# Optimization experiments

Hardware: AMD Instinct MI355X
Metric: run time of the kernel (lower is better)

The kernel has to match this reference:

```python
import jax, jax.numpy as jnp
import numpy as np

B, L, S, D, H, NS, NSLOT = 2, 2048, 2048, 1024, 16, 8, 512
HD = D // H


def _silu(x):
    return x * jax.nn.sigmoid(x)


def _layernorm(x, g, b, eps=1e-5):
    mu = jnp.mean(x, axis=-1, keepdims=True)
    var = jnp.var(x, axis=-1, keepdims=True)
    return (x - mu) * jax.lax.rsqrt(var + eps) * g + b


def setup_inputs() -> dict:
    key = jax.random.key(0)
    ks = jax.random.split(key, 12)
    x_q = jax.random.normal(ks[0], (B, L, D), dtype=jnp.float32)
    x_idx = jax.random.randint(ks[1], (B, S), 0, NSLOT)
    E_slots = jax.random.normal(ks[2], (NSLOT, D), dtype=jnp.float32)
    # EMA decay rates close to 1 so multi-scale gates stay non-degenerate over S steps
    rhos = 1.0 - 0.005 * jax.random.uniform(ks[3], (NS,), dtype=jnp.float32)
    C_seq = jax.random.uniform(ks[4], (B, L, NS), dtype=jnp.float32)
    s = 1.0 / np.sqrt(D)
    Wq = jax.random.normal(ks[5], (D, D), dtype=jnp.float32) * s
    Wk = jax.random.normal(ks[6], (D, D), dtype=jnp.float32) * s
    Wv = jax.random.normal(ks[7], (D, D), dtype=jnp.float32) * s
    Wo = jax.random.normal(ks[8], (D, D), dtype=jnp.float32) * s
    Wpe = jax.random.normal(ks[9], (D, NS), dtype=jnp.float32) * (1.0 / np.sqrt(NS))
    ln_kv_g = jnp.ones((D,), jnp.float32); ln_kv_b = jnp.zeros((D,), jnp.float32)
    ln_q_g = jnp.ones((D,), jnp.float32); ln_q_b = jnp.zeros((D,), jnp.float32)
    return dict(x_q=x_q, x_idx=x_idx, E_slots=E_slots, rhos=rhos, C_seq=C_seq,
                Wq=Wq, Wk=Wk, Wv=Wv, Wo=Wo, Wpe=Wpe,
                ln_kv_g=ln_kv_g, ln_kv_b=ln_kv_b, ln_q_g=ln_q_g, ln_q_b=ln_q_b)


def reference(x_q, x_idx, E_slots, rhos, C_seq, Wq, Wk, Wv, Wo, Wpe,
              ln_kv_g, ln_kv_b, ln_q_g, ln_q_b):
    # --- KV side: memory = ln_kv(E_slots); K/V = proj(memory); gather by slot id ---
    mem = _layernorm(E_slots, ln_kv_g, ln_kv_b)          # [NSLOT, D]
    Ek = mem @ Wk.T                                       # [NSLOT, D]
    Ev = mem @ Wv.T
    K = Ek[x_idx]                                         # [B, S, D] embedding lookup
    V = Ev[x_idx]
    # --- multiplicative EMA gate per kv position: c[s,m] = rho_m^(age) ---
    ages = (S - 1 - jnp.arange(S)).astype(x_q.dtype)      # [S]
    c_kv = jnp.power(rhos[None, :], ages[:, None])        # [S, NS]
    gate_kv = _silu(c_kv @ Wpe.T)                         # [S, D] = SiLU(pe_proj(C))
    K = K * gate_kv[None]
    V = V * gate_kv[None]
    # --- symmetric query gating: Q = q_proj(ln_q(x_q * SiLU(pe_proj(C_seq)))) ---
    gate_q = _silu(C_seq @ Wpe.T)                         # [B, L, D]
    Q = _layernorm(x_q * gate_q, ln_q_g, ln_q_b) @ Wq.T   # [B, L, D]
    # --- multi-head softmax attention ---
    q = Q.reshape(B, L, H, HD)
    k = K.reshape(B, S, H, HD)
    v = V.reshape(B, S, H, HD)
    scores = jnp.einsum('blhd,bshd->bhls', q, k) / np.sqrt(HD).astype(np.float32)
    attn = jax.nn.softmax(scores, axis=-1)                # [B, H, L, S]
    out = jnp.einsum('bhls,bshd->blhd', attn, v).reshape(B, L, D)
    return out @ Wo.T                                     # o_proj (dropout = identity, eval)
```

## Files before the change

kernel.cpp:

```cpp
#include <hip/hip_runtime.h>
#include <cmath>
#include <cstddef>

namespace {

constexpr int cB = 2, cL = 2048, cS = 2048, cD = 1024, cH = 16, cNS = 8, cNSLOT = 512, cHD = 64;

typedef __attribute__((ext_vector_type(8))) short short8;
typedef __attribute__((ext_vector_type(4))) float f32x4;

#define MFMA16(a, b, c) __builtin_amdgcn_mfma_f32_16x16x32_bf16((a), (b), (c), 0, 0, 0)

__device__ __forceinline__ float sigmoidf_(float x) { return 1.f / (1.f + __expf(-x)); }

__device__ __forceinline__ unsigned short f2bf(float x) {
  union { float f; unsigned u; } c; c.f = x;
  unsigned r = c.u + 0x7FFFu + ((c.u >> 16) & 1u);
  return (unsigned short)(r >> 16);
}
__device__ __forceinline__ float bf2f(unsigned short h) {
  union { unsigned u; float f; } c; c.u = ((unsigned)h) << 16;
  return c.f;
}

__device__ __forceinline__ void async16(const void* g, void* l) {
  __builtin_amdgcn_global_load_lds((const __attribute__((address_space(1))) void*)g,
                                   (__attribute__((address_space(3))) void*)l, 16, 0, 0);
}

__global__ __launch_bounds__(256) void prep_all_kernel(
    const float* __restrict__ Wq, const float* __restrict__ Wk,
    const float* __restrict__ Wv, const float* __restrict__ Wo,
    unsigned short* __restrict__ Wqh, unsigned short* __restrict__ Wql,
    unsigned short* __restrict__ Wkh, unsigned short* __restrict__ Wkl,
    unsigned short* __restrict__ Wvh, unsigned short* __restrict__ Wvl,
    unsigned short* __restrict__ Woh, unsigned short* __restrict__ Wol,
    const float* __restrict__ E, const float* __restrict__ lnkv_g,
    const float* __restrict__ lnkv_b, unsigned short* __restrict__ mh,
    unsigned short* __restrict__ ml, const float* __restrict__ rhos,
    const float* __restrict__ Wpe, float* __restrict__ gkv,
    const float* __restrict__ xq, const float* __restrict__ Cseq,
    const float* __restrict__ lnq_g, const float* __restrict__ lnq_b,
    unsigned short* __restrict__ Yh, unsigned short* __restrict__ Yl) {
  __shared__ float sC[cNS];
  __shared__ float rbuf[8];
  const int bid = blockIdx.x;
  const int tid = threadIdx.x;

  if (bid < 2048) {
    const int wid = bid >> 9;
    const size_t off = ((size_t)(bid & 511) * 256 + tid) * 8;
    const float* src = wid == 0 ? Wq : wid == 1 ? Wk : wid == 2 ? Wv : Wo;
    unsigned short* dh = wid == 0 ? Wqh : wid == 1 ? Wkh : wid == 2 ? Wvh : Woh;
    unsigned short* dl = wid == 0 ? Wql : wid == 1 ? Wkl : wid == 2 ? Wvl : Wol;
    const float4 a = *(const float4*)(src + off);
    const float4 b = *(const float4*)(src + off + 4);
    float v[8] = {a.x, a.y, a.z, a.w, b.x, b.y, b.z, b.w};
    unsigned short h8[8], l8[8];
#pragma unroll
    for (int j = 0; j < 8; j++) {
      h8[j] = f2bf(v[j]);
      l8[j] = f2bf(v[j] - bf2f(h8[j]));
    }
    *(uint4*)(dh + off) = *(uint4*)h8;
    *(uint4*)(dl + off) = *(uint4*)l8;
  } else if (bid < 2560) {
    const int row = bid - 2048;
    const int d0 = tid * 4;
    const float4 x = *(const float4*)(E + (size_t)row * cD + d0);
    float s1 = x.x + x.y + x.z + x.w;
    float s2 = x.x * x.x + x.y * x.y + x.z * x.z + x.w * x.w;
#pragma unroll
    for (int o = 32; o > 0; o >>= 1) { s1 += __shfl_xor(s1, o, 64); s2 += __shfl_xor(s2, o, 64); }
    if ((tid & 63) == 0) { rbuf[tid >> 6] = s1; rbuf[4 + (tid >> 6)] = s2; }
    __syncthreads();
    s1 = rbuf[0] + rbuf[1] + rbuf[2] + rbuf[3];
    s2 = rbuf[4] + rbuf[5] + rbuf[6] + rbuf[7];
    const float mean = s1 * (1.f / cD);
    const float var = s2 * (1.f / cD) - mean * mean;
    const float inv = rsqrtf(var + 1e-5f);
    const float4 g = *(const float4*)(lnkv_g + d0);
    const float4 b = *(const float4*)(lnkv_b + d0);
    float y[4];
    y[0] = (x.x - mean) * inv * g.x + b.x;
    y[1] = (x.y - mean) * inv * g.y + b.y;
    y[2] = (x.z - mean) * inv * g.z + b.z;
    y[3] = (x.w - mean) * inv * g.w + b.w;
    unsigned short h4[4], l4[4];
#pragma unroll
    for (int j = 0; j < 4; j++) {
      h4[j] = f2bf(y[j]);
      l4[j] = f2bf(y[j] - bf2f(h4[j]));
    }
    *(uint2*)(mh + (size_t)row * cD + d0) = *(uint2*)h4;
    *(uint2*)(ml + (size_t)row * cD + d0) = *(uint2*)l4;
  } else if (bid < 4608) {
    const int s = bid - 2560;
    if (tid < cNS) {
      const float age = (float)(cS - 1 - s);
      sC[tid] = __expf(age * __logf(rhos[tid]));
    }
    __syncthreads();
    const int d0 = tid * 4;
    float4 o4;
#pragma unroll
    for (int j = 0; j < 4; j++) {
      const float* wr = Wpe + (size_t)(d0 + j) * cNS;
      float gs = 0.f;
#pragma unroll
      for (int m = 0; m < cNS; m++) gs += sC[m] * wr[m];
      ((float*)&o4)[j] = gs * sigmoidf_(gs);
    }
    *(float4*)(gkv + (size_t)s * cD + d0) = o4;
  } else {
    const int row = bid - 4608;
    if (tid < cNS) sC[tid] = Cseq[(size_t)row * cNS + tid];
    __syncthreads();
    const int d0 = tid * 4;
    const float4 x = *(const float4*)(xq + (size_t)row * cD + d0);
    float y[4];
    float s1 = 0.f, s2 = 0.f;
#pragma unroll
    for (int j = 0; j < 4; j++) {
      const float* wr = Wpe + (size_t)(d0 + j) * cNS;
      float gs = 0.f;
#pragma unroll
      for (int m = 0; m < cNS; m++) gs += sC[m] * wr[m];
      const float val = ((const float*)&x)[j] * gs * sigmoidf_(gs);
      y[j] = val;
      s1 += val;
      s2 += val * val;
    }
#pragma unroll
    for (int o = 32; o > 0; o >>= 1) { s1 += __shfl_xor(s1, o, 64); s2 += __shfl_xor(s2, o, 64); }
    if ((tid & 63) == 0) { rbuf[tid >> 6] = s1; rbuf[4 + (tid >> 6)] = s2; }
    __syncthreads();
    s1 = rbuf[0] + rbuf[1] + rbuf[2] + rbuf[3];
    s2 = rbuf[4] + rbuf[5] + rbuf[6] + rbuf[7];
    const float mean = s1 * (1.f / cD);
    const float var = s2 * (1.f / cD) - mean * mean;
    const float inv = rsqrtf(var + 1e-5f);
    const float4 g = *(const float4*)(lnq_g + d0);
    const float4 b = *(const float4*)(lnq_b + d0);
    float z[4];
    z[0] = (y[0] - mean) * inv * g.x + b.x;
    z[1] = (y[1] - mean) * inv * g.y + b.y;
    z[2] = (y[2] - mean) * inv * g.z + b.z;
    z[3] = (y[3] - mean) * inv * g.w + b.w;
    unsigned short h4[4], l4[4];
#pragma unroll
    for (int j = 0; j < 4; j++) {
      h4[j] = f2bf(z[j]);
      l4[j] = f2bf(z[j] - bf2f(h4[j]));
    }
    *(uint2*)(Yh + (size_t)row * cD + d0) = *(uint2*)h4;
    *(uint2*)(Yl + (size_t)row * cD + d0) = *(uint2*)l4;
  }
}

template <int MODE>
__global__ __launch_bounds__(256, 2) void gemm_sp_kernel(
    const unsigned short* __restrict__ Ahi, const unsigned short* __restrict__ Alo,
    const unsigned short* __restrict__ Whi0, const unsigned short* __restrict__ Wlo0,
    const unsigned short* __restrict__ Whi1, const unsigned short* __restrict__ Wlo1,
    float* __restrict__ Cf0, float* __restrict__ Cf1,
    unsigned short* __restrict__ Chi,
    int M, int N, int K, float scale) {
  __shared__ __align__(16) unsigned short sAh[2][128 * 32];
  __shared__ __align__(16) unsigned short sAl[2][128 * 32];
  __shared__ __align__(16) unsigned short sBh[2][64 * 32];
  __shared__ __align__(16) unsigned short sBl[2][64 * 32];
  const unsigned short* Whi = blockIdx.z ? Whi1 : Whi0;
  const unsigned short* Wlo = blockIdx.z ? Wlo1 : Wlo0;
  float* Cf = blockIdx.z ? Cf1 : Cf0;
  const int tid = threadIdx.x;
  const int wave = tid >> 6, lane = tid & 63;
  const int quad = lane >> 4, l16 = lane & 15;
  const int m0 = blockIdx.y * 128, n0 = blockIdx.x * 64;
  const int wy = wave >> 1, wx = wave & 1;
  const int sg = (lane & 3) ^ ((lane >> 3) & 3);
  const int srow = lane >> 2;

  f32x4 acc[4][2];
#pragma unroll
  for (int i = 0; i < 4; i++)
#pragma unroll
    for (int j = 0; j < 2; j++) acc[i][j] = (f32x4){0.f, 0.f, 0.f, 0.f};

  auto stage = [&](int buf, int k0) {
#pragma unroll
    for (int c = 0; c < 2; c++) {
      const int row = c * 64 + wave * 16 + srow;
      const size_t ga = (size_t)(m0 + row) * K + k0 + sg * 8;
      async16(Ahi + ga, &sAh[buf][(c * 64 + wave * 16) * 32]);
      async16(Alo + ga, &sAl[buf][(c * 64 + wave * 16) * 32]);
    }
    const int rowb = wave * 16 + srow;
    const size_t gb = (size_t)(n0 + rowb) * K + k0 + sg * 8;
    async16(Whi + gb, &sBh[buf][wave * 16 * 32]);
    async16(Wlo + gb, &sBl[buf][wave * 16 * 32]);
  };

  stage(0, 0);
  __syncthreads();
  const int aswz = (l16 >> 1) & 3;
  int buf = 0;
  for (int k0 = 0; k0 < K; k0 += 32, buf ^= 1) {
    if (k0 + 32 < K) stage(buf ^ 1, k0 + 32);
    short8 bh[2], bl2[2];
#pragma unroll
    for (int tj = 0; tj < 2; tj++) {
      const int br = (wx * 32 + tj * 16 + l16) * 32 + ((quad ^ aswz) * 8);
      bh[tj] = *(const short8*)&sBh[buf][br];
      bl2[tj] = *(const short8*)&sBl[buf][br];
    }
#pragma unroll
    for (int ti = 0; ti < 4; ti++) {
      const int ar = (wy * 64 + ti * 16 + l16) * 32 + ((quad ^ aswz) * 8);
      const short8 ah = *(const short8*)&sAh[buf][ar];
      const short8 al2 = *(const short8*)&sAl[buf][ar];
#pragma unroll
      for (int tj = 0; tj < 2; tj++) {
        acc[ti][tj] = MFMA16(ah, bh[tj], acc[ti][tj]);
        acc[ti][tj] = MFMA16(al2, bh[tj], acc[ti][tj]);
        acc[ti][tj] = MFMA16(ah, bl2[tj], acc[ti][tj]);
      }
    }
    __syncthreads();
  }

#pragma unroll
  for (int ti = 0; ti < 4; ti++)
#pragma unroll
    for (int tj = 0; tj < 2; tj++) {
      const int row = m0 + wy * 64 + ti * 16 + quad * 4;
      const int col = n0 + wx * 32 + tj * 16 + l16;
#pragma unroll
      for (int r = 0; r < 4; r++) {
        const size_t idx = (size_t)(row + r) * N + col;
        if constexpr (MODE == 0) {
          Cf[idx] = acc[ti][tj][r];
        } else {
          Chi[idx] = f2bf(acc[ti][tj][r] * scale);
        }
      }
    }
}

__global__ __launch_bounds__(256) void prep_kv_kernel(
    const float* __restrict__ Ek, const float* __restrict__ Ev,
    const float* __restrict__ gkv, const int* __restrict__ xidx,
    unsigned short* __restrict__ Khi, unsigned short* __restrict__ Vthi) {
  __shared__ float tile[64][65];
  const int bid = blockIdx.x;
  const int tid = threadIdx.x;
  if (bid < 2048) {
    const int t = bid * 256 + tid;
    const int d0 = (t & 127) * 8;
    const int s = (t >> 7) & (cS - 1);
    const int b = t >> 18;
    const int slot = xidx[b * cS + s];
    const float4 e0 = *(const float4*)(Ek + (size_t)slot * cD + d0);
    const float4 e1 = *(const float4*)(Ek + (size_t)slot * cD + d0 + 4);
    const float4 g0 = *(const float4*)(gkv + (size_t)s * cD + d0);
    const float4 g1 = *(const float4*)(gkv + (size_t)s * cD + d0 + 4);
    float v[8] = {e0.x * g0.x, e0.y * g0.y, e0.z * g0.z, e0.w * g0.w,
                  e1.x * g1.x, e1.y * g1.y, e1.z * g1.z, e1.w * g1.w};
    unsigned short h8[8];
#pragma unroll
    for (int j = 0; j < 8; j++) h8[j] = f2bf(v[j]);
    *(uint4*)(Khi + (size_t)(b * cS + s) * cD + d0) = *(uint4*)h8;
  } else {
    const int local = bid - 2048;
    const int s0 = (local & 31) * 64;
    const int d0 = ((local >> 5) & 15) * 64;
    const int b = local >> 9;
    const int sl = tid >> 4;
    const int dl = (tid & 15) * 4;
#pragma unroll
    for (int it = 0; it < 4; it++) {
      const int s = s0 + sl + it * 16;
      const int slot = xidx[b * cS + s];
      const float4 e = *(const float4*)(Ev + (size_t)slot * cD + d0 + dl);
      const float4 g = *(const float4*)(gkv + (size_t)s * cD + d0 + dl);
      tile[sl + it * 16][dl + 0] = e.x * g.x;
      tile[sl + it * 16][dl + 1] = e.y * g.y;
      tile[sl + it * 16][dl + 2] = e.z * g.z;
      tile[sl + it * 16][dl + 3] = e.w * g.w;
    }
    __syncthreads();
    const int dr = tid >> 3;
    const int sc = (tid & 7) * 8;
#pragma unroll
    for (int it = 0; it < 2; it++) {
      const int d = d0 + dr + it * 32;
      unsigned short h8[8];
#pragma unroll
      for (int j = 0; j < 8; j++) h8[j] = f2bf(tile[sc + j][dr + it * 32]);
      *(uint4*)(Vthi + (size_t)(b * cD + d) * cS + s0 + sc) = *(uint4*)h8;
    }
  }
}

__global__ __launch_bounds__(256, 4) void attn_mfma_kernel(
    const unsigned short* __restrict__ qhi,
    const unsigned short* __restrict__ Khi,
    const unsigned short* __restrict__ Vthi,
    unsigned short* __restrict__ AOhi, unsigned short* __restrict__ AOlo) {
  __shared__ __align__(16) unsigned short sKh[64 * 64];
  __shared__ __align__(16) unsigned short sVh[64 * 64];
  __shared__ __align__(16) unsigned short sP[4][16][72];

  const int tid = threadIdx.x;
  const int wave = tid >> 6, lane = tid & 63;
  const int quad = lane >> 4, l16 = lane & 15;
  const int lB = blockIdx.x * 64;
  const int h = blockIdx.y, b = blockIdx.z;

  short8 qh[2];
  {
    const size_t base = (size_t)(b * cL + lB + wave * 16 + l16) * cD + h * cHD + quad * 8;
    qh[0] = *(const short8*)(qhi + base);
    qh[1] = *(const short8*)(qhi + base + 32);
  }

  short8 ones;
#pragma unroll
  for (int i = 0; i < 8; i++) ones[i] = (short)0x3F80;

  f32x4 O[4], dacc;
#pragma unroll
  for (int i = 0; i < 4; i++) O[i] = (f32x4){0.f, 0.f, 0.f, 0.f};
  dacc = (f32x4){0.f, 0.f, 0.f, 0.f};

  const int srow8 = lane >> 3;
  const int sg = (lane & 7) ^ srow8;

  const int r0 = (wave * 2 + 0) * 8 + srow8;
  const int r1 = (wave * 2 + 1) * 8 + srow8;
  const size_t kb0 = (size_t)(b * cS + r0) * cD + h * cHD + sg * 8;
  const size_t kb1 = (size_t)(b * cS + r1) * cD + h * cHD + sg * 8;
  const size_t vb0 = (size_t)(b * cD + h * cHD + r0) * cS + sg * 8;
  const size_t vb1 = (size_t)(b * cD + h * cHD + r1) * cS + sg * 8;

  uint4 k0h, v0h, k1h, v1h;
  k0h = *(const uint4*)(Khi + kb0);
  v0h = *(const uint4*)(Vthi + vb0);
  k1h = *(const uint4*)(Khi + kb1);
  v1h = *(const uint4*)(Vthi + vb1);

  const int j0 = wave * 2, j1 = wave * 2 + 1;

  for (int s0 = 0; s0 < cS; s0 += 64) {
    __syncthreads();
    *(uint4*)&sKh[j0 * 512 + lane * 8] = k0h;
    *(uint4*)&sVh[j0 * 512 + lane * 8] = v0h;
    *(uint4*)&sKh[j1 * 512 + lane * 8] = k1h;
    *(uint4*)&sVh[j1 * 512 + lane * 8] = v1h;
    __syncthreads();

    {
      const int sn = (s0 + 64) & (cS - 1);
      const size_t kc = (size_t)sn * cD;
      k0h = *(const uint4*)(Khi + kb0 + kc);
      v0h = *(const uint4*)(Vthi + vb0 + sn);
      k1h = *(const uint4*)(Khi + kb1 + kc);
      v1h = *(const uint4*)(Vthi + vb1 + sn);
    }

    f32x4 sc[4];
#pragma unroll
    for (int st = 0; st < 4; st++) sc[st] = (f32x4){0.f, 0.f, 0.f, 0.f};
#pragma unroll
    for (int st = 0; st < 4; st++) {
      const int srw = st * 16 + l16;
#pragma unroll
      for (int ks = 0; ks < 2; ks++) {
        const int slot = (ks * 4 + quad) ^ (srw & 7);
        const short8 kfh = *(const short8*)&sKh[srw * 64 + slot * 8];
        sc[st] = MFMA16(qh[ks], kfh, sc[st]);
      }
    }

#pragma unroll
    for (int st = 0; st < 4; st++)
#pragma unroll
      for (int r = 0; r < 4; r++)
        sP[wave][quad * 4 + r][st * 16 + l16] = f2bf(__builtin_amdgcn_exp2f(sc[st][r]));

    short8 pfh[2];
    pfh[0] = *(const short8*)&sP[wave][l16][quad * 8];
    pfh[1] = *(const short8*)&sP[wave][l16][32 + quad * 8];

#pragma unroll
    for (int dt = 0; dt < 4; dt++) {
      const int drw = dt * 16 + l16;
#pragma unroll
      for (int ss = 0; ss < 2; ss++) {
        const int slot = (ss * 4 + quad) ^ (drw & 7);
        const short8 vfh = *(const short8*)&sVh[drw * 64 + slot * 8];
        O[dt] = MFMA16(pfh[ss], vfh, O[dt]);
      }
    }
    dacc = MFMA16(pfh[0], ones, dacc);
    dacc = MFMA16(pfh[1], ones, dacc);
  }

  float inv[4];
#pragma unroll
  for (int r = 0; r < 4; r++) inv[r] = 1.f / dacc[r];
#pragma unroll
  for (int dt = 0; dt < 4; dt++)
#pragma unroll
    for (int r = 0; r < 4; r++) {
      const float v = O[dt][r] * inv[r];
      const unsigned short hi = f2bf(v);
      const size_t l = (size_t)(b * cL + lB + wave * 16 + quad * 4 + r);
      const size_t idx = l * cD + h * cHD + dt * 16 + l16;
      AOhi[idx] = hi;
      AOlo[idx] = f2bf(v - bf2f(hi));
    }
}

}

extern "C" void kernel_launch(void* const* d_in, const int* in_sizes, int n_in,
                              void* d_out, int out_size, void* d_ws, size_t ws_size,
                              hipStream_t stream) {
  (void)in_sizes; (void)n_in; (void)out_size; (void)ws_size;
  const float* x_q = (const float*)d_in[0];
  const int* x_idx = (const int*)d_in[1];
  const float* E_slots = (const float*)d_in[2];
  const float* rhos = (const float*)d_in[3];
  const float* C_seq = (const float*)d_in[4];
  const float* Wq = (const float*)d_in[5];
  const float* Wk = (const float*)d_in[6];
  const float* Wv = (const float*)d_in[7];
  const float* Wo = (const float*)d_in[8];
  const float* Wpe = (const float*)d_in[9];
  const float* ln_kv_g = (const float*)d_in[10];
  const float* ln_kv_b = (const float*)d_in[11];
  const float* ln_q_g = (const float*)d_in[12];
  const float* ln_q_b = (const float*)d_in[13];
  float* out = (float*)d_out;

  float* ws = (float*)d_ws;
  unsigned short* memhi = (unsigned short*)(ws + 0);
  unsigned short* memlo = (unsigned short*)(ws + 262144);
  unsigned short* Wkhi = (unsigned short*)(ws + 524288);
  unsigned short* Wklo = (unsigned short*)(ws + 1048576);
  unsigned short* Wvhi = (unsigned short*)(ws + 1572864);
  unsigned short* Wvlo = (unsigned short*)(ws + 2097152);
  float* gkv = ws + 2621440;
  unsigned short* qhi = (unsigned short*)(ws + 0);
  unsigned short* Wqhi = (unsigned short*)(ws + 4718592);
  unsigned short* Wqlo = (unsigned short*)(ws + 5242880);
  unsigned short* Wohi = (unsigned short*)(ws + 5767168);
  unsigned short* Wolo = (unsigned short*)(ws + 6291456);
  float* Ek = ws + 6815744;
  float* Ev = ws + 7340032;
  unsigned short* Yhi = (unsigned short*)(ws + 7864320);
  unsigned short* Ylo = (unsigned short*)(ws + 9961472);
  unsigned short* AOhi = (unsigned short*)(ws + 7864320);
  unsigned short* AOlo = (unsigned short*)(ws + 9961472);
  unsigned short* Khi = (unsigned short*)(ws + 12058624);
  unsigned short* Vthi = (unsigned short*)(ws + 16252928);

  constexpr float kQScale = 0.125f * 1.44269504088896340736f;

  prep_all_kernel<<<8704, 256, 0, stream>>>(
      Wq, Wk, Wv, Wo, Wqhi, Wqlo, Wkhi, Wklo, Wvhi, Wvlo, Wohi, Wolo,
      E_slots, ln_kv_g, ln_kv_b, memhi, memlo, rhos, Wpe, gkv,
      x_q, C_seq, ln_q_g, ln_q_b, Yhi, Ylo);
  gemm_sp_kernel<0><<<dim3(16, 4, 2), 256, 0, stream>>>(
      memhi, memlo, Wkhi, Wklo, Wvhi, Wvlo, Ek, Ev, nullptr, cNSLOT, cD, cD, 1.f);
  prep_kv_kernel<<<3072, 256, 0, stream>>>(Ek, Ev, gkv, x_idx, Khi, Vthi);
  gemm_sp_kernel<1><<<dim3(16, 32, 1), 256, 0, stream>>>(
      Yhi, Ylo, Wqhi, Wqlo, Wqhi, Wqlo, nullptr, nullptr, qhi, cB * cL, cD, cD, kQScale);
  attn_mfma_kernel<<<dim3(cL / 64, cH, cB), 256, 0, stream>>>(qhi, Khi, Vthi, AOhi, AOlo);
  gemm_sp_kernel<0><<<dim3(16, 32, 1), 256, 0, stream>>>(
      AOhi, AOlo, Wohi, Wolo, Wohi, Wolo, out, out, nullptr, cB * cL, cD, cD, 1.f);
}
```

Measured before the change: 296.1 us.

## Drop activation low-part split in GEMMs and double query rows per attention wave

Activations (layernormed memory, Q input, attention output) are now stored only as a bf16 high part. The GEMMs drop the A-low operand: one fewer MFMA per tile, half the A staging traffic and less LDS. The attention kernel now processes 32 query rows per wave (128 per block), reusing each K/V LDS fragment for two query tiles, with occupancy lowered to 2. Accuracy falls because activations lose the error-compensation term.

```diff
diff --git a/kernel.cpp b/kernel.cpp
--- a/kernel.cpp
+++ b/kernel.cpp
@@ -37,11 +37,11 @@
     unsigned short* __restrict__ Woh, unsigned short* __restrict__ Wol,
     const float* __restrict__ E, const float* __restrict__ lnkv_g,
     const float* __restrict__ lnkv_b, unsigned short* __restrict__ mh,
-    unsigned short* __restrict__ ml, const float* __restrict__ rhos,
+    const float* __restrict__ rhos,
     const float* __restrict__ Wpe, float* __restrict__ gkv,
     const float* __restrict__ xq, const float* __restrict__ Cseq,
     const float* __restrict__ lnq_g, const float* __restrict__ lnq_b,
-    unsigned short* __restrict__ Yh, unsigned short* __restrict__ Yl) {
+    unsigned short* __restrict__ Yh) {
   __shared__ float sC[cNS];
   __shared__ float rbuf[8];
   const int bid = blockIdx.x;
@@ -81,19 +81,12 @@
     const float inv = rsqrtf(var + 1e-5f);
     const float4 g = *(const float4*)(lnkv_g + d0);
     const float4 b = *(const float4*)(lnkv_b + d0);
-    float y[4];
-    y[0] = (x.x - mean) * inv * g.x + b.x;
-    y[1] = (x.y - mean) * inv * g.y + b.y;
-    y[2] = (x.z - mean) * inv * g.z + b.z;
-    y[3] = (x.w - mean) * inv * g.w + b.w;
-    unsigned short h4[4], l4[4];
-#pragma unroll
-    for (int j = 0; j < 4; j++) {
-      h4[j] = f2bf(y[j]);
-      l4[j] = f2bf(y[j] - bf2f(h4[j]));
-    }
+    unsigned short h4[4];
+    h4[0] = f2bf((x.x - mean) * inv * g.x + b.x);
+    h4[1] = f2bf((x.y - mean) * inv * g.y + b.y);
+    h4[2] = f2bf((x.z - mean) * inv * g.z + b.z);
+    h4[3] = f2bf((x.w - mean) * inv * g.w + b.w);
     *(uint2*)(mh + (size_t)row * cD + d0) = *(uint2*)h4;
-    *(uint2*)(ml + (size_t)row * cD + d0) = *(uint2*)l4;
   } else if (bid < 4608) {
     const int s = bid - 2560;
     if (tid < cNS) {
@@ -142,32 +135,24 @@
     const float inv = rsqrtf(var + 1e-5f);
     const float4 g = *(const float4*)(lnq_g + d0);
     const float4 b = *(const float4*)(lnq_b + d0);
-    float z[4];
-    z[0] = (y[0] - mean) * inv * g.x + b.x;
-    z[1] = (y[1] - mean) * inv * g.y + b.y;
-    z[2] = (y[2] - mean) * inv * g.z + b.z;
-    z[3] = (y[3] - mean) * inv * g.w + b.w;
-    unsigned short h4[4], l4[4];
-#pragma unroll
-    for (int j = 0; j < 4; j++) {
-      h4[j] = f2bf(z[j]);
-      l4[j] = f2bf(z[j] - bf2f(h4[j]));
-    }
+    unsigned short h4[4];
+    h4[0] = f2bf((y[0] - mean) * inv * g.x + b.x);
+    h4[1] = f2bf((y[1] - mean) * inv * g.y + b.y);
+    h4[2] = f2bf((y[2] - mean) * inv * g.z + b.z);
+    h4[3] = f2bf((y[3] - mean) * inv * g.w + b.w);
     *(uint2*)(Yh + (size_t)row * cD + d0) = *(uint2*)h4;
-    *(uint2*)(Yl + (size_t)row * cD + d0) = *(uint2*)l4;
   }
 }
 
 template <int MODE>
-__global__ __launch_bounds__(256, 2) void gemm_sp_kernel(
-    const unsigned short* __restrict__ Ahi, const unsigned short* __restrict__ Alo,
+__global__ __launch_bounds__(256, 2) void gemm2_kernel(
+    const unsigned short* __restrict__ Ahi,
     const unsigned short* __restrict__ Whi0, const unsigned short* __restrict__ Wlo0,
     const unsigned short* __restrict__ Whi1, const unsigned short* __restrict__ Wlo1,
     float* __restrict__ Cf0, float* __restrict__ Cf1,
     unsigned short* __restrict__ Chi,
     int M, int N, int K, float scale) {
-  __shared__ __align__(16) unsigned short sAh[2][128 * 32];
-  __shared__ __align__(16) unsigned short sAl[2][128 * 32];
+  __shared__ __align__(16) unsigned short sA[2][128 * 32];
   __shared__ __align__(16) unsigned short sBh[2][64 * 32];
   __shared__ __align__(16) unsigned short sBl[2][64 * 32];
   const unsigned short* Whi = blockIdx.z ? Whi1 : Whi0;
@@ -192,8 +177,7 @@
     for (int c = 0; c < 2; c++) {
       const int row = c * 64 + wave * 16 + srow;
       const size_t ga = (size_t)(m0 + row) * K + k0 + sg * 8;
-      async16(Ahi + ga, &sAh[buf][(c * 64 + wave * 16) * 32]);
-      async16(Alo + ga, &sAl[buf][(c * 64 + wave * 16) * 32]);
+      async16(Ahi + ga, &sA[buf][(c * 64 + wave * 16) * 32]);
     }
     const int rowb = wave * 16 + srow;
     const size_t gb = (size_t)(n0 + rowb) * K + k0 + sg * 8;
@@ -217,12 +201,10 @@
 #pragma unroll
     for (int ti = 0; ti < 4; ti++) {
       const int ar = (wy * 64 + ti * 16 + l16) * 32 + ((quad ^ aswz) * 8);
-      const short8 ah = *(const short8*)&sAh[buf][ar];
-      const short8 al2 = *(const short8*)&sAl[buf][ar];
+      const short8 ah = *(const short8*)&sA[buf][ar];
 #pragma unroll
       for (int tj = 0; tj < 2; tj++) {
         acc[ti][tj] = MFMA16(ah, bh[tj], acc[ti][tj]);
-        acc[ti][tj] = MFMA16(al2, bh[tj], acc[ti][tj]);
         acc[ti][tj] = MFMA16(ah, bl2[tj], acc[ti][tj]);
       }
     }
@@ -302,36 +284,41 @@
   }
 }
 
-__global__ __launch_bounds__(256, 4) void attn_mfma_kernel(
+__global__ __launch_bounds__(256, 2) void attn_mfma_kernel(
     const unsigned short* __restrict__ qhi,
     const unsigned short* __restrict__ Khi,
     const unsigned short* __restrict__ Vthi,
-    unsigned short* __restrict__ AOhi, unsigned short* __restrict__ AOlo) {
+    unsigned short* __restrict__ AOhi) {
   __shared__ __align__(16) unsigned short sKh[64 * 64];
   __shared__ __align__(16) unsigned short sVh[64 * 64];
-  __shared__ __align__(16) unsigned short sP[4][16][72];
+  __shared__ __align__(16) unsigned short sP[4][2][16][76];
 
   const int tid = threadIdx.x;
   const int wave = tid >> 6, lane = tid & 63;
   const int quad = lane >> 4, l16 = lane & 15;
-  const int lB = blockIdx.x * 64;
+  const int lB = blockIdx.x * 128;
   const int h = blockIdx.y, b = blockIdx.z;
 
-  short8 qh[2];
-  {
-    const size_t base = (size_t)(b * cL + lB + wave * 16 + l16) * cD + h * cHD + quad * 8;
-    qh[0] = *(const short8*)(qhi + base);
-    qh[1] = *(const short8*)(qhi + base + 32);
+  short8 qh[2][2];
+#pragma unroll
+  for (int t = 0; t < 2; t++) {
+    const size_t base =
+        (size_t)(b * cL + lB + wave * 32 + t * 16 + l16) * cD + h * cHD + quad * 8;
+    qh[t][0] = *(const short8*)(qhi + base);
+    qh[t][1] = *(const short8*)(qhi + base + 32);
   }
 
   short8 ones;
 #pragma unroll
   for (int i = 0; i < 8; i++) ones[i] = (short)0x3F80;
 
-  f32x4 O[4], dacc;
-#pragma unroll
-  for (int i = 0; i < 4; i++) O[i] = (f32x4){0.f, 0.f, 0.f, 0.f};
-  dacc = (f32x4){0.f, 0.f, 0.f, 0.f};
+  f32x4 O[2][4], dacc[2];
+#pragma unroll
+  for (int t = 0; t < 2; t++) {
+#pragma unroll
+    for (int i = 0; i < 4; i++) O[t][i] = (f32x4){0.f, 0.f, 0.f, 0.f};
+    dacc[t] = (f32x4){0.f, 0.f, 0.f, 0.f};
+  }
 
   const int srow8 = lane >> 3;
   const int sg = (lane & 7) ^ srow8;
@@ -368,9 +355,11 @@
       v1h = *(const uint4*)(Vthi + vb1 + sn);
     }
 
-    f32x4 sc[4];
-#pragma unroll
-    for (int st = 0; st < 4; st++) sc[st] = (f32x4){0.f, 0.f, 0.f, 0.f};
+    f32x4 sc[2][4];
+#pragma unroll
+    for (int t = 0; t < 2; t++)
+#pragma unroll
+      for (int st = 0; st < 4; st++) sc[t][st] = (f32x4){0.f, 0.f, 0.f, 0.f};
 #pragma unroll
     for (int st = 0; st < 4; st++) {
       const int srw = st * 16 + l16;
@@ -378,19 +367,26 @@
       for (int ks = 0; ks < 2; ks++) {
         const int slot = (ks * 4 + quad) ^ (srw & 7);
         const short8 kfh = *(const short8*)&sKh[srw * 64 + slot * 8];
-        sc[st] = MFMA16(qh[ks], kfh, sc[st]);
+        sc[0][st] = MFMA16(qh[0][ks], kfh, sc[0][st]);
+        sc[1][st] = MFMA16(qh[1][ks], kfh, sc[1][st]);
       }
     }
 
 #pragma unroll
-    for (int st = 0; st < 4; st++)
-#pragma unroll
-      for (int r = 0; r < 4; r++)
-        sP[wave][quad * 4 + r][st * 16 + l16] = f2bf(__builtin_amdgcn_exp2f(sc[st][r]));
-
-    short8 pfh[2];
-    pfh[0] = *(const short8*)&sP[wave][l16][quad * 8];
-    pfh[1] = *(const short8*)&sP[wave][l16][32 + quad * 8];
+    for (int t = 0; t < 2; t++)
+#pragma unroll
+      for (int st = 0; st < 4; st++)
+#pragma unroll
+        for (int r = 0; r < 4; r++)
+          sP[wave][t][quad * 4 + r][st * 16 + l16] =
+              f2bf(__builtin_amdgcn_exp2f(sc[t][st][r]));
+
+    short8 pfh[2][2];
+#pragma unroll
+    for (int t = 0; t < 2; t++) {
+      pfh[t][0] = *(const short8*)&sP[wave][t][l16][quad * 8];
+      pfh[t][1] = *(const short8*)&sP[wave][t][l16][32 + quad * 8];
+    }
 
 #pragma unroll
     for (int dt = 0; dt < 4; dt++) {
@@ -399,27 +395,30 @@
       for (int ss = 0; ss < 2; ss++) {
         const int slot = (ss * 4 + quad) ^ (drw & 7);
         const short8 vfh = *(const short8*)&sVh[drw * 64 + slot * 8];
-        O[dt] = MFMA16(pfh[ss], vfh, O[dt]);
+        O[0][dt] = MFMA16(pfh[0][ss], vfh, O[0][dt]);
+        O[1][dt] = MFMA16(pfh[1][ss], vfh, O[1][dt]);
       }
     }
-    dacc = MFMA16(pfh[0], ones, dacc);
-    dacc = MFMA16(pfh[1], ones, dacc);
-  }
-
-  float inv[4];
-#pragma unroll
-  for (int r = 0; r < 4; r++) inv[r] = 1.f / dacc[r];
-#pragma unroll
-  for (int dt = 0; dt < 4; dt++)
-#pragma unroll
-    for (int r = 0; r < 4; r++) {
-      const float v = O[dt][r] * inv[r];
-      const unsigned short hi = f2bf(v);
-      const size_t l = (size_t)(b * cL + lB + wave * 16 + quad * 4 + r);
-      const size_t idx = l * cD + h * cHD + dt * 16 + l16;
-      AOhi[idx] = hi;
-      AOlo[idx] = f2bf(v - bf2f(hi));
-    }
+#pragma unroll
+    for (int t = 0; t < 2; t++) {
+      dacc[t] = MFMA16(pfh[t][0], ones, dacc[t]);
+      dacc[t] = MFMA16(pfh[t][1], ones, dacc[t]);
+    }
+  }
+
+#pragma unroll
+  for (int t = 0; t < 2; t++) {
+    float inv[4];
+#pragma unroll
+    for (int r = 0; r < 4; r++) inv[r] = 1.f / dacc[t][r];
+#pragma unroll
+    for (int dt = 0; dt < 4; dt++)
+#pragma unroll
+      for (int r = 0; r < 4; r++) {
+        const size_t l = (size_t)(b * cL + lB + wave * 32 + t * 16 + quad * 4 + r);
+        AOhi[l * cD + h * cHD + dt * 16 + l16] = f2bf(O[t][dt][r] * inv[r]);
+      }
+  }
 }
 
 }
@@ -446,38 +445,35 @@
 
   float* ws = (float*)d_ws;
   unsigned short* memhi = (unsigned short*)(ws + 0);
-  unsigned short* memlo = (unsigned short*)(ws + 262144);
-  unsigned short* Wkhi = (unsigned short*)(ws + 524288);
-  unsigned short* Wklo = (unsigned short*)(ws + 1048576);
-  unsigned short* Wvhi = (unsigned short*)(ws + 1572864);
-  unsigned short* Wvlo = (unsigned short*)(ws + 2097152);
-  float* gkv = ws + 2621440;
-  unsigned short* qhi = (unsigned short*)(ws + 0);
-  unsigned short* Wqhi = (unsigned short*)(ws + 4718592);
-  unsigned short* Wqlo = (unsigned short*)(ws + 5242880);
-  unsigned short* Wohi = (unsigned short*)(ws + 5767168);
-  unsigned short* Wolo = (unsigned short*)(ws + 6291456);
-  float* Ek = ws + 6815744;
-  float* Ev = ws + 7340032;
-  unsigned short* Yhi = (unsigned short*)(ws + 7864320);
-  unsigned short* Ylo = (unsigned short*)(ws + 9961472);
-  unsigned short* AOhi = (unsigned short*)(ws + 7864320);
-  unsigned short* AOlo = (unsigned short*)(ws + 9961472);
-  unsigned short* Khi = (unsigned short*)(ws + 12058624);
-  unsigned short* Vthi = (unsigned short*)(ws + 16252928);
+  unsigned short* Wkhi = (unsigned short*)(ws + 262144);
+  unsigned short* Wklo = (unsigned short*)(ws + 786432);
+  unsigned short* Wvhi = (unsigned short*)(ws + 1310720);
+  unsigned short* Wvlo = (unsigned short*)(ws + 1835008);
+  float* gkv = ws + 2359296;
+  unsigned short* Wqhi = (unsigned short*)(ws + 4456448);
+  unsigned short* Wqlo = (unsigned short*)(ws + 4980736);
+  unsigned short* Wohi = (unsigned short*)(ws + 5505024);
+  unsigned short* Wolo = (unsigned short*)(ws + 6029312);
+  float* Ek = ws + 6553600;
+  float* Ev = ws + 7077888;
+  unsigned short* Yhi = (unsigned short*)(ws + 7602176);
+  unsigned short* AOhi = (unsigned short*)(ws + 7602176);
+  unsigned short* qhi = (unsigned short*)(ws + 9699328);
+  unsigned short* Khi = (unsigned short*)(ws + 11796480);
+  unsigned short* Vthi = (unsigned short*)(ws + 13893632);
 
   constexpr float kQScale = 0.125f * 1.44269504088896340736f;
 
   prep_all_kernel<<<8704, 256, 0, stream>>>(
       Wq, Wk, Wv, Wo, Wqhi, Wqlo, Wkhi, Wklo, Wvhi, Wvlo, Wohi, Wolo,
-      E_slots, ln_kv_g, ln_kv_b, memhi, memlo, rhos, Wpe, gkv,
-      x_q, C_seq, ln_q_g, ln_q_b, Yhi, Ylo);
-  gemm_sp_kernel<0><<<dim3(16, 4, 2), 256, 0, stream>>>(
-      memhi, memlo, Wkhi, Wklo, Wvhi, Wvlo, Ek, Ev, nullptr, cNSLOT, cD, cD, 1.f);
+      E_slots, ln_kv_g, ln_kv_b, memhi, rhos, Wpe, gkv,
+      x_q, C_seq, ln_q_g, ln_q_b, Yhi);
+  gemm2_kernel<0><<<dim3(16, 4, 2), 256, 0, stream>>>(
+      memhi, Wkhi, Wklo, Wvhi, Wvlo, Ek, Ev, nullptr, cNSLOT, cD, cD, 1.f);
   prep_kv_kernel<<<3072, 256, 0, stream>>>(Ek, Ev, gkv, x_idx, Khi, Vthi);
-  gemm_sp_kernel<1><<<dim3(16, 32, 1), 256, 0, stream>>>(
-      Yhi, Ylo, Wqhi, Wqlo, Wqhi, Wqlo, nullptr, nullptr, qhi, cB * cL, cD, cD, kQScale);
-  attn_mfma_kernel<<<dim3(cL / 64, cH, cB), 256, 0, stream>>>(qhi, Khi, Vthi, AOhi, AOlo);
-  gemm_sp_kernel<0><<<dim3(16, 32, 1), 256, 0, stream>>>(
-      AOhi, AOlo, Wohi, Wolo, Wohi, Wolo, out, out, nullptr, cB * cL, cD, cD, 1.f);
-}
+  gemm2_kernel<1><<<dim3(16, 32, 1), 256, 0, stream>>>(
+      Yhi, Wqhi, Wqlo, Wqhi, Wqlo, nullptr, nullptr, qhi, cB * cL, cD, cD, kQScale);
+  attn_mfma_kernel<<<dim3(cL / 128, cH, cB), 256, 0, stream>>>(qhi, Khi, Vthi, AOhi);
+  gemm2_kernel<0><<<dim3(16, 32, 1), 256, 0, stream>>>(
+      AOhi, Wohi, Wolo, Wohi, Wolo, out, out, nullptr, cB * cL, cD, cD, 1.f);
+}
```

Result: faster. 267.4 us (-9.7%).
